# Kernel tuning notes

Hardware: AMD Instinct MI355X
Metric: run time of the kernel (lower is better)

The kernel has to match this reference:

```python
import jax, jax.numpy as jnp
import numpy as np

EMBED_DIM = 768
HIDDEN_DIM = 384          # max(embed_dim // 2, 128)
NUM_HEADS = 12
HEAD_DIM = EMBED_DIM // NUM_HEADS
LAYER_VOCAB = 4           # len(target_layers)
THRESHOLD = 0.5
MIN_KEEP_RATIO = 0.1
B, N = 8, 1024


def setup_inputs() -> dict:
    key = jax.random.key(0)
    ks = jax.random.split(key, 12)
    std = 0.02
    return {
        "tokens": jax.random.normal(ks[0], (B, N, EMBED_DIM), jnp.float32),
        "layer_token_idx": 1,
        # actor params
        "layer_emb": jax.random.normal(ks[1], (LAYER_VOCAB, EMBED_DIM), jnp.float32) * std,
        "ln_g": jnp.ones((EMBED_DIM,), jnp.float32),
        "ln_b": jnp.zeros((EMBED_DIM,), jnp.float32),
        "w1": jax.random.normal(ks[2], (HIDDEN_DIM, EMBED_DIM), jnp.float32) * std,
        "b1": jnp.zeros((HIDDEN_DIM,), jnp.float32),
        "w2": jax.random.normal(ks[3], (HIDDEN_DIM, HIDDEN_DIM), jnp.float32) * std,
        "b2": jnp.zeros((HIDDEN_DIM,), jnp.float32),
        "w3": jax.random.normal(ks[4], (1, HIDDEN_DIM), jnp.float32) * std,
        "b3": jnp.zeros((1,), jnp.float32),
        # attention params (timm-style)
        "qkv_w": jax.random.normal(ks[5], (3 * EMBED_DIM, EMBED_DIM), jnp.float32) * std,
        "qkv_b": jnp.zeros((3 * EMBED_DIM,), jnp.float32),
        "proj_w": jax.random.normal(ks[6], (EMBED_DIM, EMBED_DIM), jnp.float32) * std,
        "proj_b": jnp.zeros((EMBED_DIM,), jnp.float32),
    }


def _layernorm(x, g, b, eps=1e-5):
    mu = x.mean(-1, keepdims=True)
    var = ((x - mu) ** 2).mean(-1, keepdims=True)
    return (x - mu) * jax.lax.rsqrt(var + eps) * g + b


def _forward(tokens, layer_token_idx, layer_emb, ln_g, ln_b, w1, b1, w2, b2, w3, b3,
             qkv_w, qkv_b, proj_w, proj_b):
    Bsz, Ntok, C = tokens.shape
    # --- MAPPOActor: logits ---
    ctx = tokens + layer_emb[layer_token_idx]               # broadcast [C]
    ctx = ctx + ctx.mean(axis=1, keepdims=True)             # global context
    h = _layernorm(ctx, ln_g, ln_b)
    h = jax.nn.gelu(h @ w1.T + b1, approximate=False)
    h = jax.nn.gelu(h @ w2.T + b2, approximate=False)
    logits = (h @ w3.T + b3).squeeze(-1)                    # [B, N]
    probs = jax.nn.sigmoid(logits)
    # --- compute_mask: threshold + min-keep topk correction ---
    binary = probs >= THRESHOLD                             # [B, N] bool
    min_keep = max(int(Ntok * MIN_KEEP_RATIO), 1)
    min_keep = min(min_keep, Ntok)
    _, topk_idx = jax.lax.top_k(probs, min_keep)            # [B, min_keep]
    fixed = jnp.zeros((Bsz, Ntok), bool).at[jnp.arange(Bsz)[:, None], topk_idx].set(True)
    need_fix = binary.sum(-1) < min_keep                    # [B]
    mask = jnp.where(need_fix[:, None], fixed, binary)
    mask = mask.at[:, 0].set(True)
    # --- masked attention (timm style) ---
    qkv = tokens @ qkv_w.T + qkv_b                          # [B, N, 3C]
    qkv = qkv.reshape(Bsz, Ntok, 3, NUM_HEADS, HEAD_DIM).transpose(2, 0, 3, 1, 4)
    q, k, v = qkv[0], qkv[1], qkv[2]                        # [B, H, N, D]
    q = q * (HEAD_DIM ** -0.5)
    scores = jnp.einsum("bhnd,bhmd->bhnm", q, k)            # [B, H, N, N]
    neg = jnp.finfo(scores.dtype).min
    scores = jnp.where(mask[:, None, None, :], scores, neg)
    attn = jax.nn.softmax(scores, axis=-1)
    v = v * mask[:, None, :, None].astype(v.dtype)
    out = jnp.einsum("bhnm,bhmd->bhnd", attn, v)
    out = out.transpose(0, 2, 1, 3).reshape(Bsz, Ntok, C)
    out = out @ proj_w.T + proj_b
    out = out * mask[..., None].astype(out.dtype)           # zero_out_queries=True
    return out


def reference(tokens, layer_token_idx, layer_emb, ln_g, ln_b, w1, b1, w2, b2, w3, b3,
              qkv_w, qkv_b, proj_w, proj_b):
    return _forward(tokens, layer_token_idx, layer_emb, ln_g, ln_b, w1, b1, w2, b2,
                    w3, b3, qkv_w, qkv_b, proj_w, proj_b)
```

## Files before the change

kernel.cpp:

```cpp
#include <hip/hip_runtime.h>
#include <cstdint>
#include <cmath>

#define EMBED 768
#define HID 384
#define NHEAD 12
#define HDIM 64
#define BATCH 8
#define NTOK 1024
#define MINKEEP 102

using f32x4  = __attribute__((ext_vector_type(4))) float;
using short8 = __attribute__((ext_vector_type(8))) short;
using short4v = __attribute__((ext_vector_type(4))) short;
using half8  = __attribute__((ext_vector_type(8))) _Float16;

__device__ inline short f2bf(float f) {
  unsigned u = __float_as_uint(f);
  u += 0x7fffu + ((u >> 16) & 1u);
  return (short)(u >> 16);
}
__device__ inline float bf2f(short s) {
  return __uint_as_float(((unsigned)(unsigned short)s) << 16);
}
__device__ inline unsigned pack_bf2(float lo, float hi) {
  unsigned ul = __float_as_uint(lo);
  ul += 0x7fffu + ((ul >> 16) & 1u);
  unsigned uh = __float_as_uint(hi);
  uh += 0x7fffu + ((uh >> 16) & 1u);
  return (ul >> 16) | (uh & 0xffff0000u);
}
__device__ inline void split2h(float v, short& h, short& m) {
  _Float16 h0 = (_Float16)v;
  float r = v - (float)h0;
  _Float16 m0 = (_Float16)r;
  h = __builtin_bit_cast(short, h0);
  m = __builtin_bit_cast(short, m0);
}

__global__ __launch_bounds__(256) void prep_kernel(
    const float* __restrict__ qkv_w, short* __restrict__ wq_bf,
    const float* __restrict__ proj_w, short* __restrict__ wp_bf,
    const float* __restrict__ w1, short* __restrict__ w1h, short* __restrict__ w1m,
    const float* __restrict__ w2, short* __restrict__ w2h, short* __restrict__ w2m,
    const float* __restrict__ tokens, float* __restrict__ colsum,
    float* __restrict__ lgt) {
  int blk = blockIdx.x, tid = threadIdx.x;
  if (blk < 2304) {
    const float* in = (blk < 1728) ? qkv_w : proj_w;
    short* out = (blk < 1728) ? wq_bf : wp_bf;
    int i = (blk < 1728 ? blk : blk - 1728) * 256 + tid;
    float4 f = ((const float4*)in)[i];
    short4v s;
    s[0] = f2bf(f.x); s[1] = f2bf(f.y); s[2] = f2bf(f.z); s[3] = f2bf(f.w);
    ((short4v*)out)[i] = s;
  } else if (blk < 2736) {
    const float* in = (blk < 2592) ? w1 : w2;
    short* oh = (blk < 2592) ? w1h : w2h;
    short* om = (blk < 2592) ? w1m : w2m;
    int i = (blk < 2592 ? blk - 2304 : blk - 2592) * 256 + tid;
    float4 f = ((const float4*)in)[i];
    short4v h, m;
    short th, tm;
    split2h(f.x, th, tm); h[0] = th; m[0] = tm;
    split2h(f.y, th, tm); h[1] = th; m[1] = tm;
    split2h(f.z, th, tm); h[2] = th; m[2] = tm;
    split2h(f.w, th, tm); h[3] = th; m[3] = tm;
    ((short4v*)oh)[i] = h;
    ((short4v*)om)[i] = m;
  } else if (blk < 2744) {
    int i = (blk - 2736) * 256 + tid;
    ((float4*)lgt)[i] = make_float4(0.f, 0.f, 0.f, 0.f);
  } else {
    int idx = blk - 2744;
    int b = idx >> 4, chunk = idx & 15;
    const float* tb = tokens + ((size_t)b * NTOK + chunk * 64) * EMBED;
    float s0 = 0.f, s1 = 0.f, s2 = 0.f;
#pragma unroll 8
    for (int n = 0; n < 64; ++n) {
      const float* r = tb + (size_t)n * EMBED;
      s0 += r[tid]; s1 += r[tid + 256]; s2 += r[tid + 512];
    }
    atomicAdd(&colsum[b * EMBED + tid], s0);
    atomicAdd(&colsum[b * EMBED + tid + 256], s1);
    atomicAdd(&colsum[b * EMBED + tid + 512], s2);
  }
}

__global__ __launch_bounds__(256) void ln_split_kernel(
    const float* __restrict__ tokens, const float* __restrict__ colsum,
    const float* __restrict__ layer_emb, const int* __restrict__ lidx,
    const float* __restrict__ gamma, const float* __restrict__ beta,
    short* __restrict__ xh, short* __restrict__ xm,
    short* __restrict__ tok_bf) {
  int row = blockIdx.x;
  int b = row >> 10;
  __shared__ float s_row[EMBED];
  __shared__ float s_red[4];
  const float* tr = tokens + (size_t)row * EMBED;
  const float* cs = colsum + b * EMBED;
  const float* eb = layer_emb + lidx[0] * EMBED;
  float lsum = 0.f;
  for (int c = threadIdx.x; c < EMBED; c += 256) {
    float t = tr[c];
    tok_bf[(size_t)row * EMBED + c] = f2bf(t);
    float v = t + 2.0f * eb[c] + cs[c] * (1.0f / NTOK);
    s_row[c] = v;
    lsum += v;
  }
  for (int o = 32; o; o >>= 1) lsum += __shfl_down(lsum, o, 64);
  int wid = threadIdx.x >> 6;
  if ((threadIdx.x & 63) == 0) s_red[wid] = lsum;
  __syncthreads();
  float mu = (s_red[0] + s_red[1] + s_red[2] + s_red[3]) * (1.f / EMBED);
  float lss = 0.f;
  for (int c = threadIdx.x; c < EMBED; c += 256) {
    float d = s_row[c] - mu;
    lss += d * d;
  }
  for (int o = 32; o; o >>= 1) lss += __shfl_down(lss, o, 64);
  __syncthreads();
  if ((threadIdx.x & 63) == 0) s_red[wid] = lss;
  __syncthreads();
  float var = (s_red[0] + s_red[1] + s_red[2] + s_red[3]) * (1.f / EMBED);
  float rinv = 1.0f / sqrtf(var + 1e-5f);
  for (int c = threadIdx.x; c < EMBED; c += 256) {
    float v = (s_row[c] - mu) * rinv * gamma[c] + beta[c];
    short h, m;
    split2h(v, h, m);
    size_t idx = (size_t)row * EMBED + c;
    xh[idx] = h; xm[idx] = m;
  }
}

__device__ inline float gelu_exact(float x) {
  return 0.5f * x * (1.0f + erff(x * 0.70710678118654752f));
}

template <int OUT>
__global__ __launch_bounds__(256) void gemm_split_kernel(
    const short* __restrict__ Ah, const short* __restrict__ Am,
    const short* __restrict__ Wh, const short* __restrict__ Wm,
    const float* __restrict__ bias, short* __restrict__ Ch,
    short* __restrict__ Cm, const float* __restrict__ w3,
    float* __restrict__ lgt, int M, int N, int K) {
  __shared__ short sA[2][64][40];
  __shared__ short sW[2][64][40];
  int tid = threadIdx.x;
  int w = tid >> 6, l = tid & 63, lg = l >> 4, lb = l & 15;
  int wr = (w >> 1) * 32, wc = (w & 1) * 32;
  int row0 = blockIdx.x * 64, col0 = blockIdx.y * 64;
  int srow = tid >> 2;
  int skk = (tid & 3) * 8;
  f32x4 acc0[2][2] = {}, acc1[2][2] = {};
  short8 ra0, ra1, rw0, rw1;
  {
    size_t aoff = (size_t)(row0 + srow) * K + skk;
    size_t woff = (size_t)(col0 + srow) * K + skk;
    ra0 = *(const short8*)(Ah + aoff);
    ra1 = *(const short8*)(Am + aoff);
    rw0 = *(const short8*)(Wh + woff);
    rw1 = *(const short8*)(Wm + woff);
  }
  for (int k0 = 0; k0 < K; k0 += 32) {
    __syncthreads();
    *(short8*)&sA[0][srow][skk] = ra0;
    *(short8*)&sA[1][srow][skk] = ra1;
    *(short8*)&sW[0][srow][skk] = rw0;
    *(short8*)&sW[1][srow][skk] = rw1;
    __syncthreads();
    if (k0 + 32 < K) {
      size_t aoff = (size_t)(row0 + srow) * K + k0 + 32 + skk;
      size_t woff = (size_t)(col0 + srow) * K + k0 + 32 + skk;
      ra0 = *(const short8*)(Ah + aoff);
      ra1 = *(const short8*)(Am + aoff);
      rw0 = *(const short8*)(Wh + woff);
      rw1 = *(const short8*)(Wm + woff);
    }
    half8 ah[2], am[2], bh[2], bm[2];
#pragma unroll
    for (int i = 0; i < 2; ++i) {
      ah[i] = *(half8*)&sA[0][wr + i * 16 + lb][lg * 8];
      am[i] = *(half8*)&sA[1][wr + i * 16 + lb][lg * 8];
      bh[i] = *(half8*)&sW[0][wc + i * 16 + lb][lg * 8];
      bm[i] = *(half8*)&sW[1][wc + i * 16 + lb][lg * 8];
    }
#pragma unroll
    for (int i = 0; i < 2; ++i)
#pragma unroll
      for (int j = 0; j < 2; ++j) {
        f32x4 c0 = acc0[i][j];
        f32x4 c1 = acc1[i][j];
        c0 = __builtin_amdgcn_mfma_f32_16x16x32_f16(ah[i], bh[j], c0, 0, 0, 0);
        c1 = __builtin_amdgcn_mfma_f32_16x16x32_f16(ah[i], bm[j], c1, 0, 0, 0);
        c0 = __builtin_amdgcn_mfma_f32_16x16x32_f16(am[i], bh[j], c0, 0, 0, 0);
        acc0[i][j] = c0;
        acc1[i][j] = c1;
      }
  }
  if (OUT == 0) {
#pragma unroll
    for (int i = 0; i < 2; ++i) {
#pragma unroll
      for (int j = 0; j < 2; ++j) {
#pragma unroll
        for (int r = 0; r < 4; ++r) {
          int grow = row0 + wr + i * 16 + lg * 4 + r;
          int gcol = col0 + wc + j * 16 + lb;
          float g = gelu_exact(acc0[i][j][r] + acc1[i][j][r] + bias[gcol]);
          size_t idx = (size_t)grow * N + gcol;
          short h, m;
          split2h(g, h, m);
          Ch[idx] = h; Cm[idx] = m;
        }
      }
    }
  } else {
    float part[2][4];
#pragma unroll
    for (int i = 0; i < 2; ++i)
#pragma unroll
      for (int r = 0; r < 4; ++r) part[i][r] = 0.f;
#pragma unroll
    for (int i = 0; i < 2; ++i) {
#pragma unroll
      for (int j = 0; j < 2; ++j) {
#pragma unroll
        for (int r = 0; r < 4; ++r) {
          int gcol = col0 + wc + j * 16 + lb;
          float g = gelu_exact(acc0[i][j][r] + acc1[i][j][r] + bias[gcol]);
          part[i][r] += g * w3[gcol];
        }
      }
    }
#pragma unroll
    for (int i = 0; i < 2; ++i) {
#pragma unroll
      for (int r = 0; r < 4; ++r) {
        float v = part[i][r];
        v += __shfl_xor(v, 1);
        v += __shfl_xor(v, 2);
        v += __shfl_xor(v, 4);
        v += __shfl_xor(v, 8);
        if (lb == 0) atomicAdd(&lgt[row0 + wr + i * 16 + lg * 4 + r], v);
      }
    }
  }
}

__global__ __launch_bounds__(1024) void mask_kernel(
    const float* __restrict__ lgt, const float* __restrict__ b3,
    int* __restrict__ kidx, int* __restrict__ kc, float* __restrict__ biasc) {
  int b = blockIdx.x, tid = threadIdx.x;
  __shared__ unsigned long long keys[1024];
  __shared__ int flag[1024];
  __shared__ int wsum[16];
  float v = lgt[b * NTOK + tid] + b3[0];
  bool bin = (v >= 0.0f);
  int wid = tid >> 6, lane = tid & 63;
  unsigned long long bal = __ballot(bin);
  if (lane == 0) wsum[wid] = __popcll(bal);
  __syncthreads();
  int total = 0;
  for (int q = 0; q < 16; ++q) total += wsum[q];
  int mv;
  if (total >= MINKEEP) {
    mv = bin ? 1 : 0;
  } else {
    flag[tid] = 0;
    unsigned u = __float_as_uint(v);
    u = (u & 0x80000000u) ? ~u : (u | 0x80000000u);
    keys[tid] = ((unsigned long long)u << 32) | (unsigned)(1023 - tid);
    __syncthreads();
    for (int k2 = 2; k2 <= 1024; k2 <<= 1) {
      for (int j = k2 >> 1; j > 0; j >>= 1) {
        int ixj = tid ^ j;
        if (ixj > tid) {
          unsigned long long a = keys[tid], c = keys[ixj];
          bool desc = ((tid & k2) == 0);
          if (desc ? (a < c) : (a > c)) {
            keys[tid] = c;
            keys[ixj] = a;
          }
        }
        __syncthreads();
      }
    }
    if (tid < MINKEEP) {
      int idx = 1023 - (int)(keys[tid] & 0xFFFFFFFFu);
      flag[idx] = 1;
    }
    __syncthreads();
    mv = flag[tid];
  }
  if (tid == 0) mv = 1;
  __syncthreads();
  unsigned long long fb = __ballot(mv != 0);
  if (lane == 0) wsum[wid] = __popcll(fb);
  __syncthreads();
  int base = 0, tot = 0;
  for (int q = 0; q < 16; ++q) {
    int vq = wsum[q];
    if (q < wid) base += vq;
    tot += vq;
  }
  int pre = base + __popcll(fb & ((1ull << lane) - 1ull));
  if (mv) {
    kidx[b * NTOK + pre] = tid;
    biasc[b * NTOK + pre] = 0.f;
  }
  if (tid >= tot) {
    kidx[b * NTOK + tid] = 0;
    biasc[b * NTOK + tid] = -3.0e38f;
  }
  if (tid == 0) kc[b] = tot;
}

__global__ __launch_bounds__(256) void qkv_gather_kernel(
    const short* __restrict__ tok_bf, const short* __restrict__ W,
    const float* __restrict__ bias, const int* __restrict__ kidx,
    const int* __restrict__ kc, short* __restrict__ qq,
    short* __restrict__ kk_, short* __restrict__ VTc) {
  __shared__ short smem[2 * 128 * 72];
  short (*sA)[72] = (short(*)[72])smem;
  short (*sW)[72] = (short(*)[72])(smem + 128 * 72);
  __shared__ int s_idx[128];
  int bx = blockIdx.x;
  int b = bx & 7, bt = bx >> 3;
  int kcb = kc[b];
  if (bt * 128 >= kcb) return;
  int tid = threadIdx.x;
  if (tid < 128) s_idx[tid] = kidx[b * NTOK + bt * 128 + tid];
  int w = tid >> 6, l = tid & 63, lg = l >> 4, lb = l & 15;
  int wr = (w >> 1) * 64, wc = (w & 1) * 64;
  int col0 = blockIdx.y * 128;
  int r_ = tid >> 3, kq = (tid & 7) * 8;
  __syncthreads();
  const short* Ab = tok_bf + (size_t)b * NTOK * EMBED;
  f32x4 acc[4][4] = {};
  short8 pa[4], pw[4];
#pragma unroll
  for (int t = 0; t < 4; ++t) {
    pa[t] = *(const short8*)(Ab + (size_t)s_idx[t * 32 + r_] * EMBED + kq);
    pw[t] = *(const short8*)(W + (size_t)(col0 + t * 32 + r_) * EMBED + kq);
  }
  for (int k0 = 0; k0 < EMBED; k0 += 64) {
    __syncthreads();
#pragma unroll
    for (int t = 0; t < 4; ++t) {
      *(short8*)&sA[t * 32 + r_][kq] = pa[t];
      *(short8*)&sW[t * 32 + r_][kq] = pw[t];
    }
    __syncthreads();
    if (k0 + 64 < EMBED) {
#pragma unroll
      for (int t = 0; t < 4; ++t) {
        pa[t] = *(const short8*)(Ab + (size_t)s_idx[t * 32 + r_] * EMBED +
                                 k0 + 64 + kq);
        pw[t] = *(const short8*)(W + (size_t)(col0 + t * 32 + r_) * EMBED +
                                 k0 + 64 + kq);
      }
    }
#pragma unroll
    for (int half = 0; half < 2; ++half) {
      short8 af[4], bfr[4];
#pragma unroll
      for (int i = 0; i < 4; ++i)
        af[i] = *(short8*)&sA[wr + i * 16 + lb][half * 32 + lg * 8];
#pragma unroll
      for (int j = 0; j < 4; ++j)
        bfr[j] = *(short8*)&sW[wc + j * 16 + lb][half * 32 + lg * 8];
#pragma unroll
      for (int i = 0; i < 4; ++i)
#pragma unroll
        for (int j = 0; j < 4; ++j)
          acc[i][j] = __builtin_amdgcn_mfma_f32_16x16x32_bf16(af[i], bfr[j],
                                                              acc[i][j], 0, 0, 0);
    }
  }
  if (col0 >= 2 * EMBED) {
    __syncthreads();
    short (*sT)[136] = (short(*)[136])smem;
#pragma unroll
    for (int i = 0; i < 4; ++i) {
#pragma unroll
      for (int j = 0; j < 4; ++j) {
        int col_local = wc + j * 16 + lb;
        int jr0 = wr + i * 16 + lg * 4;
        short4v v4;
#pragma unroll
        for (int r = 0; r < 4; ++r)
          v4[r] = f2bf(acc[i][j][r] + bias[col0 + col_local]);
        *(short4v*)&sT[col_local][jr0] = v4;
      }
    }
    __syncthreads();
    int rem = col0 - 2 * EMBED;
#pragma unroll
    for (int t = 0; t < 8; ++t) {
      int c = tid + t * 256;
      int rowl = c >> 4;
      int off = (c & 15) * 8;
      int vcol = rem + rowl;
      int h = vcol >> 6, d = vcol & 63;
      size_t dst = ((size_t)(b * NHEAD + h) * HDIM + d) * NTOK + bt * 128 + off;
      *(short8*)(VTc + dst) = *(short8*)&sT[rowl][off];
    }
    return;
  }
#pragma unroll
  for (int i = 0; i < 4; ++i) {
#pragma unroll
    for (int j = 0; j < 4; ++j) {
#pragma unroll
      for (int r = 0; r < 4; ++r) {
        int jrow = bt * 128 + wr + i * 16 + lg * 4 + r;
        int gcol = col0 + wc + j * 16 + lb;
        float val = acc[i][j][r] + bias[gcol];
        int which = gcol / EMBED;
        int rem2 = gcol - which * EMBED;
        int h = rem2 >> 6, d = rem2 & 63;
        size_t dst = ((size_t)(b * NHEAD + h) * NTOK + jrow) * HDIM + d;
        if (which == 0)
          qq[dst] = f2bf(val * 0.125f);
        else
          kk_[dst] = f2bf(val);
      }
    }
  }
}

#define ATTN_SWZ(row, colbyte) (((row)*128) + ((colbyte) ^ (((row)&7) << 4)))

__global__ __launch_bounds__(256) void attn_mfma3_kernel(
    const short* __restrict__ Qc, const short* __restrict__ Kc,
    const short* __restrict__ VTc, const float* __restrict__ biasc,
    const int* __restrict__ kc, short* __restrict__ ao) {
  __shared__ __align__(16) short sK[64 * 64];
  __shared__ __align__(16) short sVT[64 * 64];
  int bid = blockIdx.x;
  int xcd = bid & 7, slot = bid >> 3;
  int bh = xcd * 12 + (slot >> 3);
  int qt = slot & 7;
  int b = bh / NHEAD;
  int kcb = kc[b];
  if (qt * 128 >= kcb) return;
  int nt = (kcb + 63) >> 6;
  int tid = threadIdx.x;
  int w = tid >> 6, l = tid & 63, lg = l >> 4, lb = l & 15;
  int n0 = qt * 128 + w * 32;
  const short* Qp = Qc + ((size_t)bh * NTOK + n0) * HDIM;
  const short* Kp = Kc + (size_t)bh * NTOK * HDIM;
  const short* Vp = VTc + (size_t)bh * HDIM * NTOK;
  const float* bp = biasc + b * NTOK;

  short8 qf[2][2];
#pragma unroll
  for (int i = 0; i < 2; ++i)
#pragma unroll
    for (int hh = 0; hh < 2; ++hh)
      qf[i][hh] = *(const short8*)(Qp + (i * 16 + lb) * HDIM + hh * 32 + lg * 8);

  f32x4 acc[2][4] = {};
  float lr[2] = {0.f, 0.f};

  int srow = tid >> 3;
  int scol = (tid & 7) * 8;
  int scolb = scol * 2;
  short8 rk0, rk1, rv0, rv1;

#define ATTN_LOADT(m0_)                                                        \
  {                                                                            \
    rk0 = *(const short8*)(Kp + (size_t)((m0_) + srow) * HDIM + scol);         \
    rk1 = *(const short8*)(Kp + (size_t)((m0_) + srow + 32) * HDIM + scol);    \
    rv0 = *(const short8*)(Vp + (size_t)srow * NTOK + (m0_) + scol);           \
    rv1 = *(const short8*)(Vp + (size_t)(srow + 32) * NTOK + (m0_) + scol);    \
  }

  ATTN_LOADT(0);
  for (int t = 0; t < nt; ++t) {
    int m0 = t * 64;
    *(short8*)((char*)sK + ATTN_SWZ(srow, scolb)) = rk0;
    *(short8*)((char*)sK + ATTN_SWZ(srow + 32, scolb)) = rk1;
    *(short8*)((char*)sVT + ATTN_SWZ(srow, scolb)) = rv0;
    *(short8*)((char*)sVT + ATTN_SWZ(srow + 32, scolb)) = rv1;
    __syncthreads();
    if (t + 1 < nt) ATTN_LOADT(m0 + 64);

    f32x4 bias4[4];
#pragma unroll
    for (int s = 0; s < 4; ++s)
      bias4[s] = *(const f32x4*)(bp + m0 + s * 16 + lg * 4);

    f32x4 S[2][4];
#pragma unroll
    for (int s = 0; s < 4; ++s) {
      short8 kf0 = *(const short8*)((const char*)sK +
                                    ATTN_SWZ(s * 16 + lb, lg * 16));
      short8 kf1 = *(const short8*)((const char*)sK +
                                    ATTN_SWZ(s * 16 + lb, 64 + lg * 16));
#pragma unroll
      for (int i = 0; i < 2; ++i) {
        f32x4 c = bias4[s];
        c = __builtin_amdgcn_mfma_f32_16x16x32_bf16(kf0, qf[i][0], c, 0, 0, 0);
        c = __builtin_amdgcn_mfma_f32_16x16x32_bf16(kf1, qf[i][1], c, 0, 0, 0);
        S[i][s] = c;
      }
    }

    unsigned pk[2][4][2];
#pragma unroll
    for (int i = 0; i < 2; ++i) {
      float rs = 0.f;
#pragma unroll
      for (int s = 0; s < 4; ++s) {
        float p0 = __expf(S[i][s][0]);
        float p1 = __expf(S[i][s][1]);
        float p2 = __expf(S[i][s][2]);
        float p3 = __expf(S[i][s][3]);
        rs += (p0 + p1) + (p2 + p3);
        pk[i][s][0] = pack_bf2(p0, p1);
        pk[i][s][1] = pack_bf2(p2, p3);
      }
      rs += __shfl_xor(rs, 16);
      rs += __shfl_xor(rs, 32);
      lr[i] += rs;
    }

    bool hi = (lg & 2) != 0;
    int srcl = ((lg & 1) * 2) * 16 + lb;
#pragma unroll
    for (int t2 = 0; t2 < 2; ++t2) {
      short8 vf[4];
#pragma unroll
      for (int u = 0; u < 4; ++u)
        vf[u] = *(const short8*)((const char*)sVT +
                                 ATTN_SWZ(u * 16 + lb, t2 * 64 + lg * 16));
#pragma unroll
      for (int i = 0; i < 2; ++i) {
        int a0 = __shfl((int)pk[i][2 * t2][0], srcl);
        int b0 = __shfl((int)pk[i][2 * t2 + 1][0], srcl);
        int a1 = __shfl((int)pk[i][2 * t2][1], srcl);
        int b1 = __shfl((int)pk[i][2 * t2 + 1][1], srcl);
        int a2 = __shfl((int)pk[i][2 * t2][0], srcl + 16);
        int b2 = __shfl((int)pk[i][2 * t2 + 1][0], srcl + 16);
        int a3 = __shfl((int)pk[i][2 * t2][1], srcl + 16);
        int b3 = __shfl((int)pk[i][2 * t2 + 1][1], srcl + 16);
        union { short8 s8; int u[4]; } pa;
        pa.u[0] = hi ? b0 : a0;
        pa.u[1] = hi ? b1 : a1;
        pa.u[2] = hi ? b2 : a2;
        pa.u[3] = hi ? b3 : a3;
#pragma unroll
        for (int u = 0; u < 4; ++u)
          acc[i][u] = __builtin_amdgcn_mfma_f32_16x16x32_bf16(pa.s8, vf[u],
                                                              acc[i][u], 0, 0, 0);
      }
    }
    __syncthreads();
  }

  int h = bh - b * NHEAD;
#pragma unroll
  for (int i = 0; i < 2; ++i) {
#pragma unroll
    for (int r = 0; r < 4; ++r) {
      float inv = 1.0f / __shfl(lr[i], lg * 4 + r);
      int j = n0 + i * 16 + lg * 4 + r;
#pragma unroll
      for (int u = 0; u < 4; ++u) {
        ao[((size_t)b * NTOK + j) * EMBED + h * HDIM + u * 16 + lb] =
            f2bf(acc[i][u][r] * inv);
      }
    }
  }
}

__global__ __launch_bounds__(256) void proj_gather_kernel(
    const short* __restrict__ A, const short* __restrict__ W,
    const float* __restrict__ bias, const int* __restrict__ kidx,
    const int* __restrict__ kc, float* __restrict__ out) {
  __shared__ short sA[128][72];
  __shared__ short sW[128][72];
  __shared__ int s_idx[128];
  int bx = blockIdx.x;
  int b = bx & 7, bt = bx >> 3;
  int kcb = kc[b];
  if (bt * 128 >= kcb) return;
  int tid = threadIdx.x;
  if (tid < 128) s_idx[tid] = kidx[b * NTOK + bt * 128 + tid];
  int w = tid >> 6, l = tid & 63, lg = l >> 4, lb = l & 15;
  int wr = (w >> 1) * 64, wc = (w & 1) * 64;
  int col0 = blockIdx.y * 128;
  int r_ = tid >> 3, kq = (tid & 7) * 8;
  const short* Ab = A + ((size_t)b * NTOK + bt * 128) * EMBED;
  f32x4 acc[4][4] = {};
  short8 pa[4], pw[4];
#pragma unroll
  for (int t = 0; t < 4; ++t) {
    pa[t] = *(const short8*)(Ab + (size_t)(t * 32 + r_) * EMBED + kq);
    pw[t] = *(const short8*)(W + (size_t)(col0 + t * 32 + r_) * EMBED + kq);
  }
  for (int k0 = 0; k0 < EMBED; k0 += 64) {
    __syncthreads();
#pragma unroll
    for (int t = 0; t < 4; ++t) {
      *(short8*)&sA[t * 32 + r_][kq] = pa[t];
      *(short8*)&sW[t * 32 + r_][kq] = pw[t];
    }
    __syncthreads();
    if (k0 + 64 < EMBED) {
#pragma unroll
      for (int t = 0; t < 4; ++t) {
        pa[t] = *(const short8*)(Ab + (size_t)(t * 32 + r_) * EMBED + k0 + 64 + kq);
        pw[t] = *(const short8*)(W + (size_t)(col0 + t * 32 + r_) * EMBED + k0 + 64 + kq);
      }
    }
#pragma unroll
    for (int half = 0; half < 2; ++half) {
      short8 af[4], bfr[4];
#pragma unroll
      for (int i = 0; i < 4; ++i)
        af[i] = *(short8*)&sA[wr + i * 16 + lb][half * 32 + lg * 8];
#pragma unroll
      for (int j = 0; j < 4; ++j)
        bfr[j] = *(short8*)&sW[wc + j * 16 + lb][half * 32 + lg * 8];
#pragma unroll
      for (int i = 0; i < 4; ++i)
#pragma unroll
        for (int j = 0; j < 4; ++j)
          acc[i][j] = __builtin_amdgcn_mfma_f32_16x16x32_bf16(af[i], bfr[j],
                                                              acc[i][j], 0, 0, 0);
    }
  }
#pragma unroll
  for (int i = 0; i < 4; ++i) {
#pragma unroll
    for (int j = 0; j < 4; ++j) {
#pragma unroll
      for (int r = 0; r < 4; ++r) {
        int jloc = wr + i * 16 + lg * 4 + r;
        int jrow = bt * 128 + jloc;
        int gcol = col0 + wc + j * 16 + lb;
        if (jrow < kcb) {
          int n = s_idx[jloc];
          out[((size_t)b * NTOK + n) * EMBED + gcol] = acc[i][j][r] + bias[gcol];
        }
      }
    }
  }
}

extern "C" void kernel_launch(void* const* d_in, const int* in_sizes, int n_in,
                              void* d_out, int out_size, void* d_ws, size_t ws_size,
                              hipStream_t stream) {
  const float* tokens   = (const float*)d_in[0];
  const int*   lidx     = (const int*)d_in[1];
  const float* layer_emb= (const float*)d_in[2];
  const float* ln_g     = (const float*)d_in[3];
  const float* ln_b     = (const float*)d_in[4];
  const float* w1       = (const float*)d_in[5];
  const float* b1       = (const float*)d_in[6];
  const float* w2       = (const float*)d_in[7];
  const float* b2       = (const float*)d_in[8];
  const float* w3       = (const float*)d_in[9];
  const float* b3       = (const float*)d_in[10];
  const float* qkv_w    = (const float*)d_in[11];
  const float* qkv_b    = (const float*)d_in[12];
  const float* proj_w   = (const float*)d_in[13];
  const float* proj_b   = (const float*)d_in[14];
  float* out = (float*)d_out;
  float* ws = (float*)d_ws;

  float* colsum = ws;
  float* lgt    = ws + 6144;
  int*   kidx   = (int*)(ws + 14336);
  float* biasc  = ws + 22528;
  int*   kc     = (int*)(ws + 30720);
  short* tok_bf = (short*)(ws + 30736);
  short* wq_bf  = (short*)(ws + 3176464);
  short* wp_bf  = (short*)(ws + 4061200);
  short* w1h = (short*)(ws + 4356112);
  short* w1m = (short*)(ws + 4503568);
  short* w2h = (short*)(ws + 4798480);
  short* w2m = (short*)(ws + 4872208);
  const size_t X0 = 5019664;
  short* xh  = (short*)(ws + X0);
  short* xm  = (short*)(ws + X0 + 3145728);
  short* h1h = (short*)(ws + X0 + 9437184);
  short* h1m = (short*)(ws + X0 + 11010048);
  short* Qc   = (short*)(ws + X0);
  short* Kc   = (short*)(ws + X0 + 3145728);
  short* VTc  = (short*)(ws + X0 + 9437184);
  short* aoc  = (short*)(ws + X0 + 12582912);

  hipMemsetAsync(d_out, 0, (size_t)out_size * sizeof(float), stream);
  hipMemsetAsync(colsum, 0, BATCH * EMBED * sizeof(float), stream);

  prep_kernel<<<dim3(2872), dim3(256), 0, stream>>>(
      qkv_w, wq_bf, proj_w, wp_bf, w1, w1h, w1m, w2, w2h, w2m,
      tokens, colsum, lgt);

  ln_split_kernel<<<dim3(BATCH * NTOK), dim3(256), 0, stream>>>(
      tokens, colsum, layer_emb, lidx, ln_g, ln_b, xh, xm, tok_bf);
  gemm_split_kernel<0><<<dim3(128, 6), dim3(256), 0, stream>>>(
      xh, xm, w1h, w1m, b1, h1h, h1m, nullptr, nullptr,
      BATCH * NTOK, HID, EMBED);
  gemm_split_kernel<1><<<dim3(128, 6), dim3(256), 0, stream>>>(
      h1h, h1m, w2h, w2m, b2, nullptr, nullptr, w3, lgt,
      BATCH * NTOK, HID, HID);
  mask_kernel<<<dim3(BATCH), dim3(1024), 0, stream>>>(lgt, b3, kidx, kc, biasc);

  qkv_gather_kernel<<<dim3(64, 18), dim3(256), 0, stream>>>(
      tok_bf, wq_bf, qkv_b, kidx, kc, Qc, Kc, VTc);
  attn_mfma3_kernel<<<dim3(768), dim3(256), 0, stream>>>(
      Qc, Kc, VTc, biasc, kc, aoc);
  proj_gather_kernel<<<dim3(64, 6), dim3(256), 0, stream>>>(
      aoc, wp_bf, proj_b, kidx, kc, out);
}
```

Measured before the change: 155.9 us.

## Halve attention query tile and fold output zeroing into projection scatter

The attention kernel now processes 64 queries per block (16 per wave) instead of 128, doubling the grid to 1536 blocks so more CUs stay busy when few tokens are kept. The mask kernel now also writes the indices of dropped tokens after the kept ones. The projection kernel uses those indices to write zeros for dropped rows, which removes the full-output hipMemsetAsync. The cost is that each K/V tile loaded into LDS is reused by half as many queries, and the extra zero-writing blocks add some work.

```diff
diff --git a/kernel.cpp b/kernel.cpp
--- a/kernel.cpp
+++ b/kernel.cpp
@@ -304,14 +304,15 @@
     if (q < wid) base += vq;
     tot += vq;
   }
-  int pre = base + __popcll(fb & ((1ull << lane) - 1ull));
   if (mv) {
+    int pre = base + __popcll(fb & ((1ull << lane) - 1ull));
     kidx[b * NTOK + pre] = tid;
     biasc[b * NTOK + pre] = 0.f;
-  }
-  if (tid >= tot) {
-    kidx[b * NTOK + tid] = 0;
-    biasc[b * NTOK + tid] = -3.0e38f;
+  } else {
+    int nbase = wid * 64 - base;
+    int npre = nbase + __popcll(~fb & ((1ull << lane) - 1ull));
+    kidx[b * NTOK + tot + npre] = tid;
+    biasc[b * NTOK + tot + npre] = -3.0e38f;
   }
   if (tid == 0) kc[b] = tot;
 }
@@ -440,29 +441,27 @@
   __shared__ __align__(16) short sVT[64 * 64];
   int bid = blockIdx.x;
   int xcd = bid & 7, slot = bid >> 3;
-  int bh = xcd * 12 + (slot >> 3);
-  int qt = slot & 7;
+  int bh = xcd * 12 + (slot >> 4);
+  int qt = slot & 15;
   int b = bh / NHEAD;
   int kcb = kc[b];
-  if (qt * 128 >= kcb) return;
+  if (qt * 64 >= kcb) return;
   int nt = (kcb + 63) >> 6;
   int tid = threadIdx.x;
   int w = tid >> 6, l = tid & 63, lg = l >> 4, lb = l & 15;
-  int n0 = qt * 128 + w * 32;
+  int n0 = qt * 64 + w * 16;
   const short* Qp = Qc + ((size_t)bh * NTOK + n0) * HDIM;
   const short* Kp = Kc + (size_t)bh * NTOK * HDIM;
   const short* Vp = VTc + (size_t)bh * HDIM * NTOK;
   const float* bp = biasc + b * NTOK;
 
-  short8 qf[2][2];
-#pragma unroll
-  for (int i = 0; i < 2; ++i)
-#pragma unroll
-    for (int hh = 0; hh < 2; ++hh)
-      qf[i][hh] = *(const short8*)(Qp + (i * 16 + lb) * HDIM + hh * 32 + lg * 8);
-
-  f32x4 acc[2][4] = {};
-  float lr[2] = {0.f, 0.f};
+  short8 qf[2];
+#pragma unroll
+  for (int hh = 0; hh < 2; ++hh)
+    qf[hh] = *(const short8*)(Qp + lb * HDIM + hh * 32 + lg * 8);
+
+  f32x4 acc[4] = {};
+  float lr = 0.f;
 
   int srow = tid >> 3;
   int scol = (tid & 7) * 8;
@@ -492,39 +491,35 @@
     for (int s = 0; s < 4; ++s)
       bias4[s] = *(const f32x4*)(bp + m0 + s * 16 + lg * 4);
 
-    f32x4 S[2][4];
+    f32x4 S[4];
 #pragma unroll
     for (int s = 0; s < 4; ++s) {
       short8 kf0 = *(const short8*)((const char*)sK +
                                     ATTN_SWZ(s * 16 + lb, lg * 16));
       short8 kf1 = *(const short8*)((const char*)sK +
                                     ATTN_SWZ(s * 16 + lb, 64 + lg * 16));
-#pragma unroll
-      for (int i = 0; i < 2; ++i) {
-        f32x4 c = bias4[s];
-        c = __builtin_amdgcn_mfma_f32_16x16x32_bf16(kf0, qf[i][0], c, 0, 0, 0);
-        c = __builtin_amdgcn_mfma_f32_16x16x32_bf16(kf1, qf[i][1], c, 0, 0, 0);
-        S[i][s] = c;
-      }
-    }
-
-    unsigned pk[2][4][2];
-#pragma unroll
-    for (int i = 0; i < 2; ++i) {
+      f32x4 c = bias4[s];
+      c = __builtin_amdgcn_mfma_f32_16x16x32_bf16(kf0, qf[0], c, 0, 0, 0);
+      c = __builtin_amdgcn_mfma_f32_16x16x32_bf16(kf1, qf[1], c, 0, 0, 0);
+      S[s] = c;
+    }
+
+    unsigned pk[4][2];
+    {
       float rs = 0.f;
 #pragma unroll
       for (int s = 0; s < 4; ++s) {
-        float p0 = __expf(S[i][s][0]);
-        float p1 = __expf(S[i][s][1]);
-        float p2 = __expf(S[i][s][2]);
-        float p3 = __expf(S[i][s][3]);
+        float p0 = __expf(S[s][0]);
+        float p1 = __expf(S[s][1]);
+        float p2 = __expf(S[s][2]);
+        float p3 = __expf(S[s][3]);
         rs += (p0 + p1) + (p2 + p3);
-        pk[i][s][0] = pack_bf2(p0, p1);
-        pk[i][s][1] = pack_bf2(p2, p3);
+        pk[s][0] = pack_bf2(p0, p1);
+        pk[s][1] = pack_bf2(p2, p3);
       }
       rs += __shfl_xor(rs, 16);
       rs += __shfl_xor(rs, 32);
-      lr[i] += rs;
+      lr += rs;
     }
 
     bool hi = (lg & 2) != 0;
@@ -536,42 +531,36 @@
       for (int u = 0; u < 4; ++u)
         vf[u] = *(const short8*)((const char*)sVT +
                                  ATTN_SWZ(u * 16 + lb, t2 * 64 + lg * 16));
-#pragma unroll
-      for (int i = 0; i < 2; ++i) {
-        int a0 = __shfl((int)pk[i][2 * t2][0], srcl);
-        int b0 = __shfl((int)pk[i][2 * t2 + 1][0], srcl);
-        int a1 = __shfl((int)pk[i][2 * t2][1], srcl);
-        int b1 = __shfl((int)pk[i][2 * t2 + 1][1], srcl);
-        int a2 = __shfl((int)pk[i][2 * t2][0], srcl + 16);
-        int b2 = __shfl((int)pk[i][2 * t2 + 1][0], srcl + 16);
-        int a3 = __shfl((int)pk[i][2 * t2][1], srcl + 16);
-        int b3 = __shfl((int)pk[i][2 * t2 + 1][1], srcl + 16);
-        union { short8 s8; int u[4]; } pa;
-        pa.u[0] = hi ? b0 : a0;
-        pa.u[1] = hi ? b1 : a1;
-        pa.u[2] = hi ? b2 : a2;
-        pa.u[3] = hi ? b3 : a3;
-#pragma unroll
-        for (int u = 0; u < 4; ++u)
-          acc[i][u] = __builtin_amdgcn_mfma_f32_16x16x32_bf16(pa.s8, vf[u],
-                                                              acc[i][u], 0, 0, 0);
-      }
+      int a0 = __shfl((int)pk[2 * t2][0], srcl);
+      int b0 = __shfl((int)pk[2 * t2 + 1][0], srcl);
+      int a1 = __shfl((int)pk[2 * t2][1], srcl);
+      int b1 = __shfl((int)pk[2 * t2 + 1][1], srcl);
+      int a2 = __shfl((int)pk[2 * t2][0], srcl + 16);
+      int b2 = __shfl((int)pk[2 * t2 + 1][0], srcl + 16);
+      int a3 = __shfl((int)pk[2 * t2][1], srcl + 16);
+      int b3 = __shfl((int)pk[2 * t2 + 1][1], srcl + 16);
+      union { short8 s8; int u[4]; } pa;
+      pa.u[0] = hi ? b0 : a0;
+      pa.u[1] = hi ? b1 : a1;
+      pa.u[2] = hi ? b2 : a2;
+      pa.u[3] = hi ? b3 : a3;
+#pragma unroll
+      for (int u = 0; u < 4; ++u)
+        acc[u] = __builtin_amdgcn_mfma_f32_16x16x32_bf16(pa.s8, vf[u],
+                                                         acc[u], 0, 0, 0);
     }
     __syncthreads();
   }
 
   int h = bh - b * NHEAD;
 #pragma unroll
-  for (int i = 0; i < 2; ++i) {
-#pragma unroll
-    for (int r = 0; r < 4; ++r) {
-      float inv = 1.0f / __shfl(lr[i], lg * 4 + r);
-      int j = n0 + i * 16 + lg * 4 + r;
-#pragma unroll
-      for (int u = 0; u < 4; ++u) {
-        ao[((size_t)b * NTOK + j) * EMBED + h * HDIM + u * 16 + lb] =
-            f2bf(acc[i][u][r] * inv);
-      }
+  for (int r = 0; r < 4; ++r) {
+    float inv = 1.0f / __shfl(lr, lg * 4 + r);
+    int j = n0 + lg * 4 + r;
+#pragma unroll
+    for (int u = 0; u < 4; ++u) {
+      ao[((size_t)b * NTOK + j) * EMBED + h * HDIM + u * 16 + lb] =
+          f2bf(acc[u][r] * inv);
     }
   }
 }
@@ -586,16 +575,29 @@
   int bx = blockIdx.x;
   int b = bx & 7, bt = bx >> 3;
   int kcb = kc[b];
-  if (bt * 128 >= kcb) return;
   int tid = threadIdx.x;
   if (tid < 128) s_idx[tid] = kidx[b * NTOK + bt * 128 + tid];
+  int col0 = blockIdx.y * 128;
+  if (bt * 128 >= kcb) {
+    __syncthreads();
+#pragma unroll
+    for (int t = 0; t < 16; ++t) {
+      int c = tid + t * 256;
+      int rowl = c >> 5;
+      int c4 = c & 31;
+      int n = s_idx[rowl];
+      ((float4*)(out + ((size_t)b * NTOK + n) * EMBED + col0))[c4] =
+          make_float4(0.f, 0.f, 0.f, 0.f);
+    }
+    return;
+  }
   int w = tid >> 6, l = tid & 63, lg = l >> 4, lb = l & 15;
   int wr = (w >> 1) * 64, wc = (w & 1) * 64;
-  int col0 = blockIdx.y * 128;
   int r_ = tid >> 3, kq = (tid & 7) * 8;
   const short* Ab = A + ((size_t)b * NTOK + bt * 128) * EMBED;
   f32x4 acc[4][4] = {};
   short8 pa[4], pw[4];
+  __syncthreads();
 #pragma unroll
   for (int t = 0; t < 4; ++t) {
     pa[t] = *(const short8*)(Ab + (size_t)(t * 32 + r_) * EMBED + kq);
@@ -642,10 +644,9 @@
         int jloc = wr + i * 16 + lg * 4 + r;
         int jrow = bt * 128 + jloc;
         int gcol = col0 + wc + j * 16 + lb;
-        if (jrow < kcb) {
-          int n = s_idx[jloc];
-          out[((size_t)b * NTOK + n) * EMBED + gcol] = acc[i][j][r] + bias[gcol];
-        }
+        int n = s_idx[jloc];
+        out[((size_t)b * NTOK + n) * EMBED + gcol] =
+            (jrow < kcb) ? (acc[i][j][r] + bias[gcol]) : 0.f;
       }
     }
   }
@@ -694,7 +695,6 @@
   short* VTc  = (short*)(ws + X0 + 9437184);
   short* aoc  = (short*)(ws + X0 + 12582912);
 
-  hipMemsetAsync(d_out, 0, (size_t)out_size * sizeof(float), stream);
   hipMemsetAsync(colsum, 0, BATCH * EMBED * sizeof(float), stream);
 
   prep_kernel<<<dim3(2872), dim3(256), 0, stream>>>(
@@ -713,7 +713,7 @@
 
   qkv_gather_kernel<<<dim3(64, 18), dim3(256), 0, stream>>>(
       tok_bf, wq_bf, qkv_b, kidx, kc, Qc, Kc, VTc);
-  attn_mfma3_kernel<<<dim3(768), dim3(256), 0, stream>>>(
+  attn_mfma3_kernel<<<dim3(1536), dim3(256), 0, stream>>>(
       Qc, Kc, VTc, biasc, kc, aoc);
   proj_gather_kernel<<<dim3(64, 6), dim3(256), 0, stream>>>(
       aoc, wp_bf, proj_b, kidx, kc, out);
```

Result: no change. 153.5 us (-1.5%).
